# Performance work log

Hardware: AMD Instinct MI355X
Metric: run time of the kernel (lower is better)

Reference implementation:

```python
import jax, jax.numpy as jnp
import numpy as np
from jax import lax

# Model dims (see init_kwargs / mamba_ssm defaults)
B_, L_, D_IN = 8, 512, 128
D_MODEL, N_LAYERS = 512, 2
EXPAND, D_STATE, D_CONV = 2, 16, 4
D_INNER = EXPAND * D_MODEL          # 1024
DT_RANK = (D_MODEL + 15) // 16      # 32


def setup_inputs() -> dict:
    key = jax.random.key(0)
    ks = iter(jax.random.split(key, 32))
    def p(shape, scale=0.02):
        return jax.random.normal(next(ks), shape, jnp.float32) * scale
    inp = {}
    inp["x"] = jax.random.normal(next(ks), (B_, L_, D_IN), jnp.float32)
    # input projection (Linear(input_dim, d_model), with bias)
    inp["proj_in_w"] = p((D_MODEL, D_IN))
    inp["proj_in_b"] = p((D_MODEL,))
    # stacked per-layer Mamba params (leading dim = N_LAYERS)
    inp["in_proj_w"] = p((N_LAYERS, 2 * D_INNER, D_MODEL))      # no bias (mamba default)
    inp["conv_w"]    = p((N_LAYERS, D_INNER, D_CONV))           # depthwise conv1d
    inp["conv_b"]    = p((N_LAYERS, D_INNER))
    inp["x_proj_w"]  = p((N_LAYERS, DT_RANK + 2 * D_STATE, D_INNER))
    inp["dt_proj_w"] = p((N_LAYERS, D_INNER, DT_RANK))
    inp["dt_proj_b"] = jnp.full((N_LAYERS, D_INNER), 0.1, jnp.float32)
    inp["A_log"]     = jnp.log(jnp.tile(jnp.arange(1, D_STATE + 1, dtype=jnp.float32), (N_LAYERS, D_INNER, 1)))
    inp["Dm"]        = jnp.ones((N_LAYERS, D_INNER), jnp.float32)
    inp["out_proj_w"] = p((N_LAYERS, D_MODEL, D_INNER))         # no bias
    # classifier head: Linear(d_model, 64) -> ReLU -> Linear(64, 1)
    inp["cls_w1"] = p((64, D_MODEL)); inp["cls_b1"] = p((64,))
    inp["cls_w2"] = p((1, 64));       inp["cls_b2"] = p((1,))
    return inp


def _mamba_block(h, in_w, cw, cb, xp_w, dt_w, dt_b, A_log, Dm, out_w):
    B, L, _ = h.shape
    xz = jnp.einsum('bld,ed->ble', h, in_w)           # (B, L, 2*d_inner)
    xi, z = jnp.split(xz, 2, axis=-1)
    # causal depthwise conv1d (pad left d_conv-1, crop to L)
    xc = xi.transpose(0, 2, 1)                         # (B, d_inner, L)
    xc = lax.conv_general_dilated(
        xc, cw[:, None, :], (1,), [(D_CONV - 1, 0)],
        feature_group_count=D_INNER,
        dimension_numbers=('NCH', 'OIH', 'NCH')) + cb[None, :, None]
    xc = jax.nn.silu(xc).transpose(0, 2, 1)            # (B, L, d_inner)
    x_dbl = jnp.einsum('bld,ed->ble', xc, xp_w)        # (B, L, dt_rank + 2*d_state)
    dt, Bm, Cm = jnp.split(x_dbl, [DT_RANK, DT_RANK + D_STATE], axis=-1)
    dt = jax.nn.softplus(jnp.einsum('blr,dr->bld', dt, dt_w) + dt_b)  # (B, L, d_inner)
    A = -jnp.exp(A_log)                                # (d_inner, d_state)

    def step(hst, ins):
        dt_t, B_t, C_t, x_t = ins                      # (B,di),(B,ds),(B,ds),(B,di)
        dA = jnp.exp(dt_t[..., None] * A)              # (B, di, ds)
        hst = dA * hst + (dt_t * x_t)[..., None] * B_t[:, None, :]
        y = jnp.einsum('bds,bs->bd', hst, C_t)
        return hst, y

    h0 = jnp.zeros((B, D_INNER, D_STATE), h.dtype)
    xs = (dt.transpose(1, 0, 2), Bm.transpose(1, 0, 2),
          Cm.transpose(1, 0, 2), xc.transpose(1, 0, 2))
    _, ys = lax.scan(step, h0, xs)                     # ys: (L, B, d_inner)
    y = ys.transpose(1, 0, 2) + xc * Dm                # skip term D*x
    y = y * jax.nn.silu(z)                             # gate
    return jnp.einsum('ble,de->bld', y, out_w)         # (B, L, d_model)


def reference(x, proj_in_w, proj_in_b, in_proj_w, conv_w, conv_b, x_proj_w,
              dt_proj_w, dt_proj_b, A_log, Dm, out_proj_w,
              cls_w1, cls_b1, cls_w2, cls_b2):
    h = jnp.einsum('bli,di->bld', x, proj_in_w) + proj_in_b
    for l in range(N_LAYERS):
        h = _mamba_block(h, in_proj_w[l], conv_w[l], conv_b[l], x_proj_w[l],
                         dt_proj_w[l], dt_proj_b[l], A_log[l], Dm[l], out_proj_w[l])
    h = h.mean(axis=1)                                 # (B, d_model); dropout = identity (eval)
    h = jax.nn.relu(h @ cls_w1.T + cls_b1)
    logits = (h @ cls_w2.T + cls_b2).squeeze(-1)       # (B,)
    return logits
```

## Files before the change

kernel.cpp:

```cpp
#include <hip/hip_runtime.h>
#include <hip/hip_bf16.h>

#define B_   8
#define L_   512
#define DIN  128
#define DM   512
#define NLAY 2
#define DI   1024
#define DS   16
#define DTR  32
#define BL   (B_ * L_)
#define KS   8
#define CL   128
#define NCH  (L_ / CL)

typedef short bf16x8 __attribute__((ext_vector_type(8)));
typedef float floatx4 __attribute__((ext_vector_type(4)));

__device__ __forceinline__ unsigned short f2bf(float f) {
    unsigned int u = __float_as_uint(f);
    unsigned int r = (u + 0x7FFF + ((u >> 16) & 1)) >> 16;
    return (unsigned short)r;
}
__device__ __forceinline__ float bf2f(unsigned short u) {
    return __uint_as_float((unsigned int)u << 16);
}

#if __has_builtin(__builtin_amdgcn_exp2f)
#define EXP2(x) __builtin_amdgcn_exp2f(x)
#else
#define EXP2(x) __expf((x) * 0.69314718056f)
#endif

__global__ __launch_bounds__(256) void cvt_all(
    const float* __restrict__ x,  unsigned short* __restrict__ xbf,
    const float* __restrict__ pw, unsigned short* __restrict__ wpin,
    const float* __restrict__ iw, unsigned short* __restrict__ win,
    const float* __restrict__ ow, unsigned short* __restrict__ wout,
    float* __restrict__ hm)
{
    int bid = blockIdx.x;
    if (bid >= 1824) {
        int i = (bid - 1824) * 2048 + threadIdx.x * 8;
        float4 z = make_float4(0.f, 0.f, 0.f, 0.f);
        *(float4*)(hm + i) = z;
        *(float4*)(hm + i + 4) = z;
        return;
    }
    const float* src; unsigned short* dst; int off;
    if      (bid < 256)  { src = x;  dst = xbf;  off = bid; }
    else if (bid < 288)  { src = pw; dst = wpin; off = bid - 256; }
    else if (bid < 1312) { src = iw; dst = win;  off = bid - 288; }
    else                 { src = ow; dst = wout; off = bid - 1312; }
    int i = (off * 256 + threadIdx.x) * 8;
    float4 a = *(const float4*)(src + i);
    float4 b = *(const float4*)(src + i + 4);
    unsigned short o[8];
    o[0] = f2bf(a.x); o[1] = f2bf(a.y); o[2] = f2bf(a.z); o[3] = f2bf(a.w);
    o[4] = f2bf(b.x); o[5] = f2bf(b.y); o[6] = f2bf(b.z); o[7] = f2bf(b.w);
    *(uint4*)(dst + i) = *(uint4*)o;
}

__global__ __launch_bounds__(256) void gemm_mfma(
    const unsigned short* __restrict__ A,
    const unsigned short* __restrict__ W,
    float* __restrict__ C, unsigned short* __restrict__ Cb,
    int N, int K)
{
    __shared__ unsigned short As[128 * 40];
    __shared__ unsigned short Ws[128 * 40];

    const int tid  = threadIdx.x;
    const int row  = tid >> 1;
    const int half = tid & 1;
    const long aBase = (long)(blockIdx.y * 128 + row) * K + half * 16;
    const long wBase = (long)(blockIdx.x * 128 + row) * K + half * 16;
    const int  lbase = row * 40 + half * 16;

    const int lane = tid & 63;
    const int wv   = tid >> 6;
    const int wm   = (wv >> 1) * 64;
    const int wn   = (wv & 1) * 64;
    const int lr   = lane & 15;
    const int q    = lane >> 4;

    floatx4 acc[4][4];
#pragma unroll
    for (int i = 0; i < 4; ++i)
#pragma unroll
        for (int j = 0; j < 4; ++j)
#pragma unroll
            for (int r = 0; r < 4; ++r) acc[i][j][r] = 0.f;

    for (int k0 = 0; k0 < K; k0 += 32) {
        __syncthreads();
        const unsigned short* ap = A + aBase + k0;
        const unsigned short* wp = W + wBase + k0;
        uint4 a0 = *(const uint4*)ap;
        uint4 a1 = *(const uint4*)(ap + 8);
        uint4 w0 = *(const uint4*)wp;
        uint4 w1 = *(const uint4*)(wp + 8);
        *(uint4*)(As + lbase)     = a0;
        *(uint4*)(As + lbase + 8) = a1;
        *(uint4*)(Ws + lbase)     = w0;
        *(uint4*)(Ws + lbase + 8) = w1;
        __syncthreads();

        bf16x8 af[4], bfr[4];
#pragma unroll
        for (int i = 0; i < 4; ++i)
            af[i] = *(const bf16x8*)(As + (wm + i * 16 + lr) * 40 + q * 8);
#pragma unroll
        for (int j = 0; j < 4; ++j)
            bfr[j] = *(const bf16x8*)(Ws + (wn + j * 16 + lr) * 40 + q * 8);
#pragma unroll
        for (int i = 0; i < 4; ++i)
#pragma unroll
            for (int j = 0; j < 4; ++j)
                acc[i][j] = __builtin_amdgcn_mfma_f32_16x16x32_bf16(
                    af[i], bfr[j], acc[i][j], 0, 0, 0);
    }

#pragma unroll
    for (int i = 0; i < 4; ++i) {
#pragma unroll
        for (int r = 0; r < 4; ++r) {
            const int  crow = blockIdx.y * 128 + wm + i * 16 + q * 4 + r;
            const long base = (long)crow * N + blockIdx.x * 128 + wn + lr;
#pragma unroll
            for (int j = 0; j < 4; ++j) {
                float v = acc[i][j][r];
                if (C)  C[base + j * 16] = v;
                if (Cb) Cb[base + j * 16] = f2bf(v);
            }
        }
    }
}

__global__ __launch_bounds__(256) void gemm_mfma_n64(
    const unsigned short* __restrict__ A,
    const unsigned short* __restrict__ W,
    const float* __restrict__ bias,
    float* __restrict__ C, unsigned short* __restrict__ Cb,
    int N, int K, int meanmode, float* __restrict__ hm)
{
    __shared__ unsigned short As[128 * 40];
    __shared__ unsigned short Ws[64 * 40];
    __shared__ float colsum[64];

    const int tid   = threadIdx.x;
    const int arow  = tid >> 1;
    const int ahalf = tid & 1;
    const long aBase = (long)(blockIdx.y * 128 + arow) * K + ahalf * 16;
    const int  albase = arow * 40 + ahalf * 16;
    const int wrow = tid >> 2;
    const int wq   = tid & 3;
    const long wBase = (long)(blockIdx.x * 64 + wrow) * K + wq * 8;
    const int  wlbase = wrow * 40 + wq * 8;

    const int lane = tid & 63;
    const int wv   = tid >> 6;
    const int wm   = wv * 32;
    const int lr   = lane & 15;
    const int q    = lane >> 4;

    floatx4 acc[2][4];
#pragma unroll
    for (int i = 0; i < 2; ++i)
#pragma unroll
        for (int j = 0; j < 4; ++j)
#pragma unroll
            for (int r = 0; r < 4; ++r) acc[i][j][r] = 0.f;

    for (int k0 = 0; k0 < K; k0 += 32) {
        __syncthreads();
        const unsigned short* ap = A + aBase + k0;
        uint4 a0 = *(const uint4*)ap;
        uint4 a1 = *(const uint4*)(ap + 8);
        uint4 w0 = *(const uint4*)(W + wBase + k0);
        *(uint4*)(As + albase)     = a0;
        *(uint4*)(As + albase + 8) = a1;
        *(uint4*)(Ws + wlbase)     = w0;
        __syncthreads();

        bf16x8 af[2], bfr[4];
#pragma unroll
        for (int i = 0; i < 2; ++i)
            af[i] = *(const bf16x8*)(As + (wm + i * 16 + lr) * 40 + q * 8);
#pragma unroll
        for (int j = 0; j < 4; ++j)
            bfr[j] = *(const bf16x8*)(Ws + (j * 16 + lr) * 40 + q * 8);
#pragma unroll
        for (int i = 0; i < 2; ++i)
#pragma unroll
            for (int j = 0; j < 4; ++j)
                acc[i][j] = __builtin_amdgcn_mfma_f32_16x16x32_bf16(
                    af[i], bfr[j], acc[i][j], 0, 0, 0);
    }

    if (meanmode) {
        if (tid < 64) colsum[tid] = 0.f;
        __syncthreads();
#pragma unroll
        for (int j = 0; j < 4; ++j) {
            float p = 0.f;
#pragma unroll
            for (int i = 0; i < 2; ++i)
#pragma unroll
                for (int r = 0; r < 4; ++r) p += acc[i][j][r];
            atomicAdd(&colsum[j * 16 + lr], p);
        }
        __syncthreads();
        if (tid < 64) {
            const int b = blockIdx.y >> 2;
            atomicAdd(&hm[b * DM + blockIdx.x * 64 + tid],
                      colsum[tid] * (1.f / (float)L_));
        }
        return;
    }

    float bj[4] = {0.f, 0.f, 0.f, 0.f};
    if (bias) {
#pragma unroll
        for (int j = 0; j < 4; ++j)
            bj[j] = bias[blockIdx.x * 64 + j * 16 + lr];
    }
#pragma unroll
    for (int i = 0; i < 2; ++i) {
#pragma unroll
        for (int r = 0; r < 4; ++r) {
            const int  crow = blockIdx.y * 128 + wm + i * 16 + q * 4 + r;
            const long base = (long)crow * N + blockIdx.x * 64 + lr;
#pragma unroll
            for (int j = 0; j < 4; ++j) {
                float v = acc[i][j][r] + bj[j];
                if (C)  C[base + j * 16] = v;
                if (Cb) Cb[base + j * 16] = f2bf(v);
            }
        }
    }
}

__global__ __launch_bounds__(256) void xprojconv(
    const unsigned short* __restrict__ xzb, const float* __restrict__ cw,
    const float* __restrict__ cb, const float* __restrict__ W,
    float* __restrict__ P, float* __restrict__ xcout)
{
    __shared__ float As[16][68];
    __shared__ float Ws[16][68];

    const int tid  = threadIdx.x;
    const int tx   = tid & 15;
    const int ty   = tid >> 4;
    const int lrow = tid >> 2;
    const int lk   = (tid & 3) << 2;
    const int kbase = blockIdx.x * (DI / KS);

    const int m = blockIdx.y * 64 + lrow;
    const int t = m & (L_ - 1);
    const float* Wp = W + lrow * DI + kbase + lk;

    float acc[4][4] = {};

    for (int k0 = 0; k0 < DI / KS; k0 += 16) {
        const int dcol = kbase + k0 + lk;
        float4 cbv = *(const float4*)(cb + dcol);
        float sums[4] = {cbv.x, cbv.y, cbv.z, cbv.w};
        float4 cwq[4];
#pragma unroll
        for (int q = 0; q < 4; ++q) cwq[q] = *(const float4*)(cw + (dcol + q) * 4);
#pragma unroll
        for (int w = 0; w < 4; ++w) {
            int tw = t - 3 + w;
            if (tw >= 0) {
                const uint2 up = *(const uint2*)(xzb + (long)(m - 3 + w) * (2 * DI) + dcol);
                float x0 = __uint_as_float(up.x << 16);
                float x1 = __uint_as_float(up.x & 0xffff0000u);
                float x2 = __uint_as_float(up.y << 16);
                float x3 = __uint_as_float(up.y & 0xffff0000u);
                sums[0] += ((const float*)&cwq[0])[w] * x0;
                sums[1] += ((const float*)&cwq[1])[w] * x1;
                sums[2] += ((const float*)&cwq[2])[w] * x2;
                sums[3] += ((const float*)&cwq[3])[w] * x3;
            }
        }
        float4 a4;
#pragma unroll
        for (int q = 0; q < 4; ++q)
            ((float*)&a4)[q] = sums[q] / (1.f + __expf(-sums[q]));
        float4 wv = *(const float4*)(Wp + k0);
        *(float4*)(xcout + (long)m * DI + dcol) = a4;

        __syncthreads();
        As[lk + 0][lrow] = a4.x; As[lk + 1][lrow] = a4.y;
        As[lk + 2][lrow] = a4.z; As[lk + 3][lrow] = a4.w;
        Ws[lk + 0][lrow] = wv.x; Ws[lk + 1][lrow] = wv.y;
        Ws[lk + 2][lrow] = wv.z; Ws[lk + 3][lrow] = wv.w;
        __syncthreads();
#pragma unroll
        for (int k = 0; k < 16; ++k) {
            const float4 a44 = *(const float4*)&As[k][ty << 2];
            const float4 w4  = *(const float4*)&Ws[k][tx << 2];
            acc[0][0] += a44.x * w4.x; acc[0][1] += a44.x * w4.y;
            acc[0][2] += a44.x * w4.z; acc[0][3] += a44.x * w4.w;
            acc[1][0] += a44.y * w4.x; acc[1][1] += a44.y * w4.y;
            acc[1][2] += a44.y * w4.z; acc[1][3] += a44.y * w4.w;
            acc[2][0] += a44.z * w4.x; acc[2][1] += a44.z * w4.y;
            acc[2][2] += a44.z * w4.z; acc[2][3] += a44.z * w4.w;
            acc[3][0] += a44.w * w4.x; acc[3][1] += a44.w * w4.y;
            acc[3][2] += a44.w * w4.z; acc[3][3] += a44.w * w4.w;
        }
    }

    float* out = P + (long)blockIdx.x * (BL * 64)
               + (blockIdx.y * 64 + (ty << 2)) * 64 + (tx << 2);
#pragma unroll
    for (int i = 0; i < 4; ++i)
        *(float4*)(out + i * 64) = make_float4(acc[i][0], acc[i][1],
                                               acc[i][2], acc[i][3]);
}

__global__ __launch_bounds__(256) void xproj_reduce(
    const float* __restrict__ P, float* __restrict__ xdbl)
{
    int i = (blockIdx.x * 256 + threadIdx.x) * 4;
    float4 s = *(const float4*)(P + i);
#pragma unroll
    for (int k = 1; k < KS; ++k) {
        float4 p = *(const float4*)(P + (long)k * (BL * 64) + i);
        s.x += p.x; s.y += p.y; s.z += p.z; s.w += p.w;
    }
    *(float4*)(xdbl + i) = s;
}

template <int CTRL>
__device__ __forceinline__ float dpp_shr_add(float v) {
    int sh = __builtin_amdgcn_update_dpp(0, __float_as_int(v), CTRL, 0xF, 0xF, true);
    return v + __int_as_float(sh);
}

__global__ __launch_bounds__(256) void scan_fused(
    const float* __restrict__ xc, const float* __restrict__ xdbl,
    const float* __restrict__ A_log, const float* __restrict__ dtw,
    const float* __restrict__ dtpb, const float* __restrict__ Dm,
    const unsigned short* __restrict__ xzb, unsigned short* __restrict__ ysb16)
{
    __shared__ float  sdtw[16][36];
    __shared__ float  sxd [CL][36];
    __shared__ float4 sdp [CL / 2][17];
    __shared__ float4 sbc4[CL / 2][17];
    __shared__ float  sy  [16][CL + 4];

    const int tid  = threadIdx.x;
    const int s    = tid & 15;
    const int grp  = tid >> 4;
    const int bd0  = blockIdx.x * 16;
    const int b    = bd0 >> 10;
    const int d0   = bd0 & (DI - 1);
    const int mb0  = b * L_;

    const int j  = tid & 15;
    const int tt = tid >> 4;

    {
        float2 w = *(const float2*)(dtw + (d0 + j) * DTR + tt * 2);
        sdtw[j][tt * 2] = w.x; sdtw[j][tt * 2 + 1] = w.y;
    }
    const float a    = -__expf(A_log[(d0 + grp) * DS + s]);
    const float bias = dtpb[d0 + j];
    const float dmv  = Dm[d0 + j];

    float  rxc[8], rB[8], rC[8], rz[8];
    float2 rxd[8];
#pragma unroll
    for (int i = 0; i < 8; ++i) {
        int m = mb0 + tt + 16 * i;
        rxc[i] = xc[m * DI + d0 + j];
        rxd[i] = *(const float2*)(xdbl + m * 64 + j * 2);
        rB[i]  = xdbl[m * 64 + DTR + j];
        rC[i]  = xdbl[m * 64 + DTR + DS + j];
        rz[i]  = bf2f(xzb[(long)m * (2 * DI) + DI + d0 + j]);
    }

    float state = 0.f;

    for (int c = 0; c < NCH; ++c) {
        const int mbase = mb0 + c * CL;
        float xcur[8], zcur[8];
#pragma unroll
        for (int i = 0; i < 8; ++i) { xcur[i] = rxc[i]; zcur[i] = rz[i]; }

        __syncthreads();
#pragma unroll
        for (int i = 0; i < 8; ++i) {
            int t = tt + 16 * i;
            *(float2*)&sxd[t][j * 2] = rxd[i];
            ((float2*)&sbc4[t >> 1][j])[t & 1] = make_float2(rB[i], rC[i]);
        }
        __syncthreads();

        if (c < NCH - 1) {
#pragma unroll
            for (int i = 0; i < 8; ++i) {
                int m = mbase + CL + tt + 16 * i;
                rxc[i] = xc[m * DI + d0 + j];
                rxd[i] = *(const float2*)(xdbl + m * 64 + j * 2);
                rB[i]  = xdbl[m * 64 + DTR + j];
                rC[i]  = xdbl[m * 64 + DTR + DS + j];
                rz[i]  = bf2f(xzb[(long)m * (2 * DI) + DI + d0 + j]);
            }
        }

        {
            float4 wreg[8];
#pragma unroll
            for (int k = 0; k < 8; ++k) wreg[k] = *(const float4*)&sdtw[j][k * 4];
#pragma unroll
            for (int i = 0; i < 8; ++i) {
                int t = tt + 16 * i;
                float acc = bias;
#pragma unroll
                for (int k = 0; k < 8; ++k) {
                    float4 xv = *(const float4*)&sxd[t][k * 4];
                    acc += xv.x * wreg[k].x + xv.y * wreg[k].y
                         + xv.z * wreg[k].z + xv.w * wreg[k].w;
                }
                float dt = (acc > 20.f) ? acc : __logf(1.f + __expf(acc));
                ((float2*)&sdp[t >> 1][j])[t & 1] =
                    make_float2(dt * 1.44269504f, dt * xcur[i]);
            }
        }
        __syncthreads();

        for (int t4 = 0; t4 < CL; t4 += 4) {
            float ybuf[4];
#pragma unroll
            for (int h = 0; h < 2; ++h) {
                const int t2 = (t4 >> 1) + h;
                const float4 dp = sdp[t2][grp];
                const float4 bc = sbc4[t2][s];
                {
                    const float dA = EXP2(dp.x * a);
                    state = fmaf(dA, state, dp.y * bc.x);
                    float contrib = state * bc.y;
                    contrib = dpp_shr_add<0x111>(contrib);
                    contrib = dpp_shr_add<0x112>(contrib);
                    contrib = dpp_shr_add<0x114>(contrib);
                    contrib = dpp_shr_add<0x118>(contrib);
                    ybuf[h * 2] = contrib;
                }
                {
                    const float dA = EXP2(dp.z * a);
                    state = fmaf(dA, state, dp.w * bc.z);
                    float contrib = state * bc.w;
                    contrib = dpp_shr_add<0x111>(contrib);
                    contrib = dpp_shr_add<0x112>(contrib);
                    contrib = dpp_shr_add<0x114>(contrib);
                    contrib = dpp_shr_add<0x118>(contrib);
                    ybuf[h * 2 + 1] = contrib;
                }
            }
            if (s == 15) *(float4*)&sy[grp][t4] = *(float4*)ybuf;
        }
        __syncthreads();

#pragma unroll
        for (int i = 0; i < 8; ++i) {
            int t = tt + 16 * i;
            float z = zcur[i];
            float sz = z / (1.f + __expf(-z));
            float val = (sy[j][t] + xcur[i] * dmv) * sz;
            ysb16[(mbase + t) * DI + d0 + j] = f2bf(val);
        }
    }
}

__global__ __launch_bounds__(512) void meancls_kernel(
    const float* __restrict__ hm, const float* __restrict__ w1,
    const float* __restrict__ b1, const float* __restrict__ w2,
    const float* __restrict__ b2, float* __restrict__ out)
{
    __shared__ float shm[DM];
    __shared__ float su[64];
    const int b = blockIdx.x, tid = threadIdx.x;
    shm[tid] = hm[b * DM + tid];
    __syncthreads();

    const int j = tid >> 3, sl = tid & 7;
    const float* wr = w1 + j * DM + sl * 64;
    const float* hb = shm + sl * 64;
    float p = 0.f;
    for (int k = 0; k < 64; k += 4)
        p += hb[k] * wr[k] + hb[k+1] * wr[k+1]
           + hb[k+2] * wr[k+2] + hb[k+3] * wr[k+3];
    p += __shfl_xor(p, 1);
    p += __shfl_xor(p, 2);
    p += __shfl_xor(p, 4);
    if (sl == 0) su[j] = fmaxf(p + b1[j], 0.f) * w2[j];
    __syncthreads();
    if (tid < 64) {
        float v = su[tid];
#pragma unroll
        for (int off = 32; off; off >>= 1) v += __shfl_down(v, off);
        if (tid == 0) out[b] = v + b2[0];
    }
}

extern "C" void kernel_launch(void* const* d_in, const int* in_sizes, int n_in,
                              void* d_out, int out_size, void* d_ws, size_t ws_size,
                              hipStream_t stream) {
    const float* x          = (const float*)d_in[0];
    const float* proj_in_w  = (const float*)d_in[1];
    const float* proj_in_b  = (const float*)d_in[2];
    const float* in_proj_w  = (const float*)d_in[3];
    const float* conv_w     = (const float*)d_in[4];
    const float* conv_b     = (const float*)d_in[5];
    const float* x_proj_w   = (const float*)d_in[6];
    const float* dt_proj_w  = (const float*)d_in[7];
    const float* dt_proj_b  = (const float*)d_in[8];
    const float* A_log      = (const float*)d_in[9];
    const float* Dm         = (const float*)d_in[10];
    const float* out_proj_w = (const float*)d_in[11];
    const float* cls_w1     = (const float*)d_in[12];
    const float* cls_b1     = (const float*)d_in[13];
    const float* cls_w2     = (const float*)d_in[14];
    const float* cls_b2     = (const float*)d_in[15];
    float* out = (float*)d_out;

    float* ws   = (float*)d_ws;
    float* h    = ws;
    float* xzf  = h    + BL * DM;
    float* xcb  = xzf  + BL * 2 * DI;
    float* xdbl = xcb  + BL * DI;
    float* scr  = xdbl + BL * 64;
    float* hm   = scr  + 2 * BL * DI;
    float* hmp  = hm   + B_ * DM;
    unsigned short* xzb  = (unsigned short*)xzf;
    unsigned short* u16  = (unsigned short*)(hmp + 64 * DM);
    unsigned short* xbf  = u16;
    unsigned short* hbf  = xbf  + BL * DIN;
    unsigned short* ysbf = hbf  + BL * DM;
    unsigned short* wpin = ysbf + BL * DI;
    unsigned short* win  = wpin + DM * DIN;
    unsigned short* wout = win  + NLAY * 2 * DI * DM;
    float* xpart = scr;

    cvt_all<<<1826, 256, 0, stream>>>(x, xbf, proj_in_w, wpin,
                                      in_proj_w, win, out_proj_w, wout, hm);

    gemm_mfma_n64<<<dim3(DM / 64, BL / 128), 256, 0, stream>>>(
        xbf, wpin, proj_in_b, nullptr, hbf, DM, DIN, 0, nullptr);

    for (int l = 0; l < NLAY; ++l) {
        gemm_mfma<<<dim3(2 * DI / 128, BL / 128), 256, 0, stream>>>(
            hbf, win + l * 2 * DI * DM, nullptr, xzb, 2 * DI, DM);
        xprojconv<<<dim3(KS, 64), 256, 0, stream>>>(
            xzb, conv_w + l * DI * 4, conv_b + l * DI,
            x_proj_w + l * 64 * DI, xpart, xcb);
        xproj_reduce<<<256, 256, 0, stream>>>(xpart, xdbl);
        scan_fused<<<(B_ * DI) / 16, 256, 0, stream>>>(
            xcb, xdbl, A_log + l * DI * DS, dt_proj_w + l * DI * DTR,
            dt_proj_b + l * DI, Dm + l * DI, xzb, ysbf);
        if (l == NLAY - 1) {
            gemm_mfma_n64<<<dim3(DM / 64, BL / 128), 256, 0, stream>>>(
                ysbf, wout + l * DM * DI, nullptr, nullptr, nullptr,
                DM, DI, 1, hm);
        } else {
            gemm_mfma_n64<<<dim3(DM / 64, BL / 128), 256, 0, stream>>>(
                ysbf, wout + l * DM * DI, nullptr, nullptr, hbf,
                DM, DI, 0, nullptr);
        }
    }

    meancls_kernel<<<B_, 512, 0, stream>>>(hm, cls_w1, cls_b1,
                                           cls_w2, cls_b2, out);
}
```

Baseline: 345.5 us.

## Stage GEMM tiles via direct global-to-LDS loads with K-step of 64

Both MFMA GEMM kernels now fill shared memory with global_load_lds, which copies straight from global memory into LDS without going through registers. The K tile grows from 32 to 64 and the row stride changes from padded 40 to unpadded 64. This halves the number of barrier pairs and removes register staging traffic. The unpadded 64-element rows can cause LDS bank conflicts on the fragment reads, and the loop has no wait on the async loads beyond __syncthreads.

```diff
diff --git a/kernel.cpp b/kernel.cpp
--- a/kernel.cpp
+++ b/kernel.cpp
@@ -32,6 +32,13 @@
 #define EXP2(x) __expf((x) * 0.69314718056f)
 #endif
 
+__device__ __forceinline__ void gld_lds16(const unsigned short* g, unsigned short* l) {
+    __builtin_amdgcn_global_load_lds(
+        (const __attribute__((address_space(1))) void*)g,
+        (__attribute__((address_space(3))) void*)l,
+        16, 0, 0);
+}
+
 __global__ __launch_bounds__(256) void cvt_all(
     const float* __restrict__ x,  unsigned short* __restrict__ xbf,
     const float* __restrict__ pw, unsigned short* __restrict__ wpin,
@@ -67,16 +74,10 @@
     float* __restrict__ C, unsigned short* __restrict__ Cb,
     int N, int K)
 {
-    __shared__ unsigned short As[128 * 40];
-    __shared__ unsigned short Ws[128 * 40];
+    __shared__ unsigned short As[128 * 64];
+    __shared__ unsigned short Ws[128 * 64];
 
     const int tid  = threadIdx.x;
-    const int row  = tid >> 1;
-    const int half = tid & 1;
-    const long aBase = (long)(blockIdx.y * 128 + row) * K + half * 16;
-    const long wBase = (long)(blockIdx.x * 128 + row) * K + half * 16;
-    const int  lbase = row * 40 + half * 16;
-
     const int lane = tid & 63;
     const int wv   = tid >> 6;
     const int wm   = (wv >> 1) * 64;
@@ -84,6 +85,11 @@
     const int lr   = lane & 15;
     const int q    = lane >> 4;
 
+    const int srow  = lane >> 3;
+    const int skcol = (lane & 7) * 8;
+    const long aRowBase = (long)blockIdx.y * 128;
+    const long wRowBase = (long)blockIdx.x * 128;
+
     floatx4 acc[4][4];
 #pragma unroll
     for (int i = 0; i < 4; ++i)
@@ -92,33 +98,35 @@
 #pragma unroll
             for (int r = 0; r < 4; ++r) acc[i][j][r] = 0.f;
 
-    for (int k0 = 0; k0 < K; k0 += 32) {
-        __syncthreads();
-        const unsigned short* ap = A + aBase + k0;
-        const unsigned short* wp = W + wBase + k0;
-        uint4 a0 = *(const uint4*)ap;
-        uint4 a1 = *(const uint4*)(ap + 8);
-        uint4 w0 = *(const uint4*)wp;
-        uint4 w1 = *(const uint4*)(wp + 8);
-        *(uint4*)(As + lbase)     = a0;
-        *(uint4*)(As + lbase + 8) = a1;
-        *(uint4*)(Ws + lbase)     = w0;
-        *(uint4*)(Ws + lbase + 8) = w1;
-        __syncthreads();
-
-        bf16x8 af[4], bfr[4];
-#pragma unroll
-        for (int i = 0; i < 4; ++i)
-            af[i] = *(const bf16x8*)(As + (wm + i * 16 + lr) * 40 + q * 8);
-#pragma unroll
-        for (int j = 0; j < 4; ++j)
-            bfr[j] = *(const bf16x8*)(Ws + (wn + j * 16 + lr) * 40 + q * 8);
-#pragma unroll
-        for (int i = 0; i < 4; ++i)
+    for (int k0 = 0; k0 < K; k0 += 64) {
+        __syncthreads();
+#pragma unroll
+        for (int c = 0; c < 4; ++c) {
+            const int chunk = wv * 4 + c;
+            const int row   = chunk * 8 + srow;
+            gld_lds16(A + (aRowBase + row) * K + k0 + skcol,
+                      As + chunk * 512 + lane * 8);
+            gld_lds16(W + (wRowBase + row) * K + k0 + skcol,
+                      Ws + chunk * 512 + lane * 8);
+        }
+        __syncthreads();
+
+#pragma unroll
+        for (int kk = 0; kk < 2; ++kk) {
+            bf16x8 af[4], bfr[4];
+#pragma unroll
+            for (int i = 0; i < 4; ++i)
+                af[i] = *(const bf16x8*)(As + (wm + i * 16 + lr) * 64 + kk * 32 + q * 8);
 #pragma unroll
             for (int j = 0; j < 4; ++j)
-                acc[i][j] = __builtin_amdgcn_mfma_f32_16x16x32_bf16(
-                    af[i], bfr[j], acc[i][j], 0, 0, 0);
+                bfr[j] = *(const bf16x8*)(Ws + (wn + j * 16 + lr) * 64 + kk * 32 + q * 8);
+#pragma unroll
+            for (int i = 0; i < 4; ++i)
+#pragma unroll
+                for (int j = 0; j < 4; ++j)
+                    acc[i][j] = __builtin_amdgcn_mfma_f32_16x16x32_bf16(
+                        af[i], bfr[j], acc[i][j], 0, 0, 0);
+        }
     }
 
 #pragma unroll
@@ -144,26 +152,22 @@
     float* __restrict__ C, unsigned short* __restrict__ Cb,
     int N, int K, int meanmode, float* __restrict__ hm)
 {
-    __shared__ unsigned short As[128 * 40];
-    __shared__ unsigned short Ws[64 * 40];
+    __shared__ unsigned short As[128 * 64];
+    __shared__ unsigned short Ws[64 * 64];
     __shared__ float colsum[64];
 
-    const int tid   = threadIdx.x;
-    const int arow  = tid >> 1;
-    const int ahalf = tid & 1;
-    const long aBase = (long)(blockIdx.y * 128 + arow) * K + ahalf * 16;
-    const int  albase = arow * 40 + ahalf * 16;
-    const int wrow = tid >> 2;
-    const int wq   = tid & 3;
-    const long wBase = (long)(blockIdx.x * 64 + wrow) * K + wq * 8;
-    const int  wlbase = wrow * 40 + wq * 8;
-
+    const int tid  = threadIdx.x;
     const int lane = tid & 63;
     const int wv   = tid >> 6;
     const int wm   = wv * 32;
     const int lr   = lane & 15;
     const int q    = lane >> 4;
 
+    const int srow  = lane >> 3;
+    const int skcol = (lane & 7) * 8;
+    const long aRowBase = (long)blockIdx.y * 128;
+    const long wRowBase = (long)blockIdx.x * 64;
+
     floatx4 acc[2][4];
 #pragma unroll
     for (int i = 0; i < 2; ++i)
@@ -172,30 +176,40 @@
 #pragma unroll
             for (int r = 0; r < 4; ++r) acc[i][j][r] = 0.f;
 
-    for (int k0 = 0; k0 < K; k0 += 32) {
-        __syncthreads();
-        const unsigned short* ap = A + aBase + k0;
-        uint4 a0 = *(const uint4*)ap;
-        uint4 a1 = *(const uint4*)(ap + 8);
-        uint4 w0 = *(const uint4*)(W + wBase + k0);
-        *(uint4*)(As + albase)     = a0;
-        *(uint4*)(As + albase + 8) = a1;
-        *(uint4*)(Ws + wlbase)     = w0;
-        __syncthreads();
-
-        bf16x8 af[2], bfr[4];
-#pragma unroll
-        for (int i = 0; i < 2; ++i)
-            af[i] = *(const bf16x8*)(As + (wm + i * 16 + lr) * 40 + q * 8);
-#pragma unroll
-        for (int j = 0; j < 4; ++j)
-            bfr[j] = *(const bf16x8*)(Ws + (j * 16 + lr) * 40 + q * 8);
-#pragma unroll
-        for (int i = 0; i < 2; ++i)
+    for (int k0 = 0; k0 < K; k0 += 64) {
+        __syncthreads();
+#pragma unroll
+        for (int c = 0; c < 4; ++c) {
+            const int chunk = wv * 4 + c;
+            const int row   = chunk * 8 + srow;
+            gld_lds16(A + (aRowBase + row) * K + k0 + skcol,
+                      As + chunk * 512 + lane * 8);
+        }
+#pragma unroll
+        for (int c = 0; c < 2; ++c) {
+            const int chunk = wv * 2 + c;
+            const int row   = chunk * 8 + srow;
+            gld_lds16(W + (wRowBase + row) * K + k0 + skcol,
+                      Ws + chunk * 512 + lane * 8);
+        }
+        __syncthreads();
+
+#pragma unroll
+        for (int kk = 0; kk < 2; ++kk) {
+            bf16x8 af[2], bfr[4];
+#pragma unroll
+            for (int i = 0; i < 2; ++i)
+                af[i] = *(const bf16x8*)(As + (wm + i * 16 + lr) * 64 + kk * 32 + q * 8);
 #pragma unroll
             for (int j = 0; j < 4; ++j)
-                acc[i][j] = __builtin_amdgcn_mfma_f32_16x16x32_bf16(
-                    af[i], bfr[j], acc[i][j], 0, 0, 0);
+                bfr[j] = *(const bf16x8*)(Ws + (j * 16 + lr) * 64 + kk * 32 + q * 8);
+#pragma unroll
+            for (int i = 0; i < 2; ++i)
+#pragma unroll
+                for (int j = 0; j < 4; ++j)
+                    acc[i][j] = __builtin_amdgcn_mfma_f32_16x16x32_bf16(
+                        af[i], bfr[j], acc[i][j], 0, 0, 0);
+        }
     }
 
     if (meanmode) {
```

After: 335.6 us. 1.03x faster.
